# Kernel tuning notes

Measured on AMD Instinct MI355X. Metric: run time of the kernel, lower is better.

## Reference

```python
import jax, jax.numpy as jnp
from jax import lax
import numpy as np

N, C, H, W = 8, 128, 96, 96
G, K = 8, 3                      # groups, kernel_size
GC = C // G                      # group channels = 16
STRIDE, PAD, DIL = 1, 1, 1
OFFSET_SCALE = 1.0
OM_DIM = int(np.ceil(G * K * K * 3 / 8) * 8)   # 216 (== G*K*K*3, no padding)
GN_EPS = 1e-5


def setup_inputs() -> dict:
    key = jax.random.key(0)
    ks = jax.random.split(key, 7)
    inp = {
        "input": jax.random.normal(ks[0], (N, C, H, W), dtype=jnp.float32),
        # depthwise conv (Conv2d groups=C): OIHW with I=1
        "dw_w": jax.random.normal(ks[1], (C, 1, K, K), dtype=jnp.float32) * 0.1,
        "dw_b": jax.random.normal(ks[2], (C,), dtype=jnp.float32) * 0.05,
        # GroupNorm(num_groups=1) affine params
        "gn_w": jnp.ones((C,), dtype=jnp.float32),
        "gn_b": jnp.zeros((C,), dtype=jnp.float32),
        # offset_mask Linear (module zero-inits; use small random for a meaningful test)
        "om_w": jax.random.normal(ks[3], (OM_DIM, C), dtype=jnp.float32) * 0.02,
        "om_b": jax.random.normal(ks[4], (OM_DIM,), dtype=jnp.float32) * 0.02,
    }
    return inp


def _dcnv4_forward(x, dw_w, dw_b, gn_w, gn_b, om_w, om_b):
    # x: (N, C, H, W)
    # ---- offset/mask branch: depthwise conv -> GroupNorm(1) -> GELU -> Linear
    x1 = lax.conv_general_dilated(
        x, dw_w, window_strides=(1, 1), padding=[(1, 1), (1, 1)],
        feature_group_count=C, dimension_numbers=("NCHW", "OIHW", "NCHW"))
    x1 = x1 + dw_b[None, :, None, None]
    mu = jnp.mean(x1, axis=(1, 2, 3), keepdims=True)
    var = jnp.var(x1, axis=(1, 2, 3), keepdims=True)
    x1 = (x1 - mu) * lax.rsqrt(var + GN_EPS)
    x1 = x1 * gn_w[None, :, None, None] + gn_b[None, :, None, None]
    x1 = jax.nn.gelu(x1, approximate=False)
    x1 = jnp.transpose(x1, (0, 2, 3, 1))                     # (N,H,W,C)
    om = jnp.einsum("nhwc,oc->nhwo", x1, om_w) + om_b        # (N,H,W,216)

    K2 = K * K
    om = om[..., : G * K2 * 3].reshape(N, H, W, G, K2 * 3)
    offs = om[..., : 2 * K2].reshape(N, H, W, G, K2, 2)      # (dx, dy) per point
    mask = om[..., 2 * K2:]                                  # (N,H,W,G,K2), no softmax in DCNv4

    # ---- sampling locations (pixel coords in the unpadded input, zeros outside)
    ky, kx = jnp.meshgrid(jnp.arange(K), jnp.arange(K), indexing="ij")
    base_y = ((ky - (K - 1) / 2.0) * DIL).reshape(-1).astype(jnp.float32)  # (K2,)
    base_x = ((kx - (K - 1) / 2.0) * DIL).reshape(-1).astype(jnp.float32)
    ctr_y = jnp.arange(H, dtype=jnp.float32) * STRIDE - PAD + DIL * (K - 1) / 2.0
    ctr_x = jnp.arange(W, dtype=jnp.float32) * STRIDE - PAD + DIL * (K - 1) / 2.0
    loc_y = ctr_y[None, :, None, None, None] + (base_y + offs[..., 1]) * OFFSET_SCALE
    loc_x = ctr_x[None, None, :, None, None] + (base_x + offs[..., 0]) * OFFSET_SCALE

    # ---- grouped bilinear gather
    xv = jnp.transpose(x, (0, 2, 3, 1)).reshape(N, H, W, G, GC)   # values, channels-last
    y0 = jnp.floor(loc_y)
    x0 = jnp.floor(loc_x)
    ly = loc_y - y0
    lx = loc_x - x0
    y0i = y0.astype(jnp.int32)
    x0i = x0.astype(jnp.int32)
    n_idx = jnp.arange(N)[:, None, None, None, None]
    g_idx = jnp.arange(G)[None, None, None, :, None]

    def gather(yi, xi):
        valid = (yi >= 0) & (yi < H) & (xi >= 0) & (xi < W)
        yc = jnp.clip(yi, 0, H - 1)
        xc = jnp.clip(xi, 0, W - 1)
        v = xv[n_idx, yc, xc, g_idx]                 # (N,H,W,G,K2,GC)
        return v * valid[..., None].astype(xv.dtype)

    samp = (gather(y0i,     x0i)     * ((1 - ly) * (1 - lx))[..., None]
          + gather(y0i,     x0i + 1) * ((1 - ly) * lx)[..., None]
          + gather(y0i + 1, x0i)     * (ly * (1 - lx))[..., None]
          + gather(y0i + 1, x0i + 1) * (ly * lx)[..., None])

    out = jnp.sum(samp * mask[..., None], axis=4)    # (N,H,W,G,GC)
    out = out.reshape(N, H, W, C)
    return jnp.transpose(out, (0, 3, 1, 2))          # (N,C,H,W)


def reference(input, dw_w, dw_b, gn_w, gn_b, om_w, om_b):
    return _dcnv4_forward(input, dw_w, dw_b, gn_w, gn_b, om_w, om_b)
```

## Files before the change

kernel.cpp:

```cpp
#include <hip/hip_runtime.h>
#include <hip/hip_bf16.h>

#define N_   8
#define C_   128
#define H_   96
#define W_   96
#define G_   8
#define GC_  16
#define HW_  (H_ * W_)
#define CHW_ (C_ * HW_)
#define OM_  216
#define OMP_ 224
#define OMROWS2_ 112
#define EPS_ 1e-5f
#define BLKS_PER_N_ 192
#define PW_  100
#define PPLANE_ (PW_ * PW_ * GC_)

typedef short bf16x8 __attribute__((ext_vector_type(8)));
typedef float f32x4 __attribute__((ext_vector_type(4)));

#if __has_builtin(__builtin_amdgcn_fdot2_f32_bf16)
#define HAVE_DOT2_ 1
typedef __bf16 bf16x2 __attribute__((ext_vector_type(2)));
static __device__ __forceinline__ bf16x2 u2bf2(unsigned int u) {
  union { unsigned int i; bf16x2 v; } c;
  c.i = u;
  return c.v;
}
#else
#define HAVE_DOT2_ 0
#endif

static __device__ __forceinline__ unsigned short f2bf(float f) {
  unsigned int u = __float_as_uint(f);
  unsigned int r = (u + 0x7fffu + ((u >> 16) & 1u)) >> 16;
  return (unsigned short)r;
}
static __device__ __forceinline__ unsigned int pk_bf2(float lo, float hi) {
  __hip_bfloat162 h = __float22bfloat162_rn(make_float2(lo, hi));
  union { __hip_bfloat162 h; unsigned int u; } c;
  c.h = h;
  return c.u;
}
static __device__ __forceinline__ float lo_bf(unsigned int u) {
  return __uint_as_float(u << 16);
}
static __device__ __forceinline__ float hi_bf(unsigned int u) {
  return __uint_as_float(u & 0xffff0000u);
}

static __device__ __forceinline__ float fast_gelu(float z) {
  float s = z * 0.70710678118654752f;
  float as = fabsf(s);
  float t = __builtin_amdgcn_rcpf(fmaf(0.3275911f, as, 1.0f));
  float e = __expf(-as * as);
  float inner = fmaf(fmaf(fmaf(fmaf(1.061405429f, t, -1.453152027f), t,
                               1.421413741f), t, -0.284496736f), t, 0.254829592f);
  float y = fmaf(-inner * t, e, 1.0f);
  float erf_s = copysignf(y, s);
  float hz = 0.5f * z;
  return fmaf(hz, erf_s, hz);
}

static __device__ __forceinline__ void loadrow5(float dst[2][5],
                                                const float* __restrict__ xp0,
                                                const float* __restrict__ xp1,
                                                int hh, int w0) {
  bool vy = (hh >= 0) & (hh < H_);
#pragma unroll
  for (int j = 0; j < 5; ++j) {
    int ww = w0 - 1 + j;
    bool v = vy & (ww >= 0) & (ww < W_);
    dst[0][j] = v ? xp0[hh * W_ + ww] : 0.0f;
    dst[1][j] = v ? xp1[hh * W_ + ww] : 0.0f;
  }
}

__global__ __launch_bounds__(256) void k_front(const float* __restrict__ x,
                                               const float* __restrict__ dw_w,
                                               const float* __restrict__ dw_b,
                                               unsigned short* __restrict__ xgb,
                                               unsigned short* __restrict__ x1b,
                                               float2* __restrict__ partials) {
  __shared__ unsigned int lds_c[384 * 9];
  __shared__ unsigned int lds_a[384 * 9];
  __shared__ float ls[4], lq[4];

  int tx = threadIdx.x;
  int ty = threadIdx.y;
  int tid = ty * 32 + tx;
  int hb = blockIdx.x;
  int g  = blockIdx.y;
  int n  = blockIdx.z;
  int h0 = hb * 4;
  int w0 = tx * 3;

  const int c0 = g * 16 + 2 * ty;
  float wk[2][9];
  const float* wp = dw_w + c0 * 9;
#pragma unroll
  for (int j = 0; j < 9; ++j) {
    wk[0][j] = wp[j];
    wk[1][j] = wp[9 + j];
  }
  float bias[2] = {dw_b[c0], dw_b[c0 + 1]};

  const float* xp0 = x + ((size_t)(n * C_ + c0)) * HW_;
  const float* xp1 = xp0 + HW_;

  float s = 0.0f, q = 0.0f;

  float rr[3][2][5];
  loadrow5(rr[0], xp0, xp1, h0 - 1, w0);
  loadrow5(rr[1], xp0, xp1, h0,     w0);

#pragma unroll
  for (int r = 0; r < 4; ++r) {
    const int sA = r % 3;
    const int sB = (r + 1) % 3;
    const int sC = (r + 2) % 3;
    loadrow5(rr[sC], xp0, xp1, h0 + r + 1, w0);

#pragma unroll
    for (int j = 0; j < 3; ++j) {
      float acc0 = bias[0], acc1 = bias[1];
#pragma unroll
      for (int dx = 0; dx < 3; ++dx) {
        acc0 = fmaf(rr[sA][0][j + dx], wk[0][0 + dx], acc0);
        acc1 = fmaf(rr[sA][1][j + dx], wk[1][0 + dx], acc1);
        acc0 = fmaf(rr[sB][0][j + dx], wk[0][3 + dx], acc0);
        acc1 = fmaf(rr[sB][1][j + dx], wk[1][3 + dx], acc1);
        acc0 = fmaf(rr[sC][0][j + dx], wk[0][6 + dx], acc0);
        acc1 = fmaf(rr[sC][1][j + dx], wk[1][6 + dx], acc1);
      }
      float cen0 = rr[sB][0][j + 1];
      float cen1 = rr[sB][1][j + 1];
      s += acc0 + acc1;
      q = fmaf(acc0, acc0, q);
      q = fmaf(acc1, acc1, q);
      int pxl = r * 96 + w0 + j;
      lds_a[pxl * 9 + ty] = pk_bf2(acc0, acc1);
      lds_c[pxl * 9 + ty] = pk_bf2(cen0, cen1);
    }
  }
  __syncthreads();

  for (int i = tid; i < 384; i += 256) {
    int row = i / 96;
    int col = i - row * 96;
    unsigned int wc[8], wa[8];
#pragma unroll
    for (int k = 0; k < 8; ++k) {
      wc[k] = lds_c[i * 9 + k];
      wa[k] = lds_a[i * 9 + k];
    }
    unsigned int* xg = (unsigned int*)xgb + (size_t)(n * G_ + g) * (PPLANE_ / 2)
                       + ((h0 + row + 2) * PW_ + (col + 2)) * 8;
    uint4 c01 = {wc[0], wc[1], wc[2], wc[3]};
    uint4 c23 = {wc[4], wc[5], wc[6], wc[7]};
    *(uint4*)xg = c01;
    *(uint4*)(xg + 4) = c23;
    int p = (h0 + row) * W_ + col;
    unsigned int* xb = (unsigned int*)x1b + ((size_t)n * HW_ + p) * 64 + g * 8;
    uint4 a01 = {wa[0], wa[1], wa[2], wa[3]};
    uint4 a23 = {wa[4], wa[5], wa[6], wa[7]};
    *(uint4*)xb = a01;
    *(uint4*)(xb + 4) = a23;
  }

#pragma unroll
  for (int o = 32; o > 0; o >>= 1) {
    s += __shfl_down(s, o);
    q += __shfl_down(q, o);
  }
  int lane = tid & 63;
  int wv = tid >> 6;
  if (lane == 0) { ls[wv] = s; lq[wv] = q; }
  __syncthreads();
  if (tid == 0) {
    int bid = hb + 24 * g + BLKS_PER_N_ * n;
    partials[bid] = make_float2(ls[0] + ls[1] + ls[2] + ls[3],
                                lq[0] + lq[1] + lq[2] + lq[3]);
  }
}

__global__ __launch_bounds__(256) void k_prep(const float* __restrict__ om_w,
                                              const float* __restrict__ om_b,
                                              unsigned short* __restrict__ A,
                                              float* __restrict__ biasp,
                                              unsigned short* __restrict__ xgb) {
  int b = blockIdx.x;
  int tid = threadIdx.x;
  if (b < 112) {
    int idx = b * 256 + tid;
    int o = idx >> 7;
    int cix = idx & 127;
    int g = o / 28;
    int k = o - g * 28;
    float v = (k < 27) ? om_w[(g * 27 + k) * C_ + cix] : 0.0f;
    A[idx] = f2bf(v);
    if (cix == 0) biasp[o] = (k < 27) ? om_b[g * 27 + k] : 0.0f;
  } else {
    int gid = (b - 112) * 256 + tid;
    const int NBORD = 64 * 784;
    for (int id = gid; id < NBORD; id += 80 * 256) {
      int plane = id / 784;
      int r = id - plane * 784;
      int row, col;
      if (r < 400) {
        int qq = r / 100;
        row = (qq < 2) ? qq : qq + 96;
        col = r - qq * 100;
      } else {
        int r2 = r - 400;
        int qq = r2 >> 2;
        int c4 = r2 & 3;
        row = 2 + qq;
        col = (c4 < 2) ? c4 : c4 + 96;
      }
      uint4* dst = (uint4*)(xgb + (size_t)plane * PPLANE_ + (row * PW_ + col) * GC_);
      uint4 z = {0, 0, 0, 0};
      dst[0] = z;
      dst[1] = z;
    }
  }
}

static __device__ __forceinline__ void pref_af(bf16x8 (&af)[4],
                                               const unsigned short* __restrict__ A,
                                               int ot, int l16, int quad) {
  const unsigned short* Ap = A + (ot * 16 + l16) * C_ + quad * 8;
#pragma unroll
  for (int kk = 0; kk < 4; ++kk) af[kk] = *(const bf16x8*)(Ap + kk * 32);
}

__global__ __launch_bounds__(256) void k_gemm_mfma(const unsigned short* __restrict__ Bt,
                                                   const unsigned short* __restrict__ A,
                                                   const float* __restrict__ biasp,
                                                   const float2* __restrict__ partials,
                                                   const float* __restrict__ gn_w,
                                                   const float* __restrict__ gn_b,
                                                   unsigned int* __restrict__ om2) {
  __shared__ unsigned short Bl[32 * 136];
  __shared__ alignas(16) float s_bias[OMP_];
  __shared__ float ls[4], lq[4];
  int tid = threadIdx.x;
  int pb = blockIdx.x;
  int n = blockIdx.y;
  int p0 = pb * 32;

  const unsigned short* src = Bt + ((size_t)n * HW_ + p0) * C_;
  int col = tid & 15;
  int row0 = tid >> 4;
  uint4 raw0 = *(const uint4*)(src + row0 * C_ + col * 8);
  uint4 raw1 = *(const uint4*)(src + (16 + row0) * C_ + col * 8);
  int cbase = col * 8;
  float gw8[8], gb8[8];
#pragma unroll
  for (int j = 0; j < 8; ++j) {
    gw8[j] = gn_w[cbase + j];
    gb8[j] = gn_b[cbase + j];
  }
  if (tid < OMP_ / 4) {
    ((float4*)s_bias)[tid] = ((const float4*)biasp)[tid];
  }

  {
    float s = 0.0f, q = 0.0f;
    if (tid < BLKS_PER_N_) {
      float2 v = partials[n * BLKS_PER_N_ + tid];
      s = v.x;
      q = v.y;
    }
#pragma unroll
    for (int o = 32; o > 0; o >>= 1) {
      s += __shfl_down(s, o);
      q += __shfl_down(q, o);
    }
    int lane = tid & 63;
    int wv = tid >> 6;
    if (lane == 0) { ls[wv] = s; lq[wv] = q; }
  }
  __syncthreads();

  float sum = ls[0] + ls[1] + ls[2] + ls[3];
  float ssq = lq[0] + lq[1] + lq[2] + lq[3];
  const float inv = 1.0f / (float)CHW_;
  float mean = sum * inv;
  float var = ssq * inv - mean * mean;
  float rstd = rsqrtf(var + EPS_);
  float a8[8], b8[8];
#pragma unroll
  for (int j = 0; j < 8; ++j) {
    a8[j] = rstd * gw8[j];
    b8[j] = gb8[j] - mean * rstd * gw8[j];
  }

  {
    uint4 raws[2] = {raw0, raw1};
#pragma unroll
    for (int i = 0; i < 2; ++i) {
      int row = row0 + i * 16;
      unsigned int d[4] = {raws[i].x, raws[i].y, raws[i].z, raws[i].w};
      unsigned int od[4];
#pragma unroll
      for (int t = 0; t < 4; ++t) {
        float v0 = lo_bf(d[t]);
        float v1 = hi_bf(d[t]);
        float z0 = fmaf(v0, a8[2 * t], b8[2 * t]);
        float z1 = fmaf(v1, a8[2 * t + 1], b8[2 * t + 1]);
        od[t] = pk_bf2(fast_gelu(z0), fast_gelu(z1));
      }
      uint4 packed = {od[0], od[1], od[2], od[3]};
      *(uint4*)(&Bl[row * 136 + col * 8]) = packed;
    }
  }
  __syncthreads();

  int wave = tid >> 6;
  int lane = tid & 63;
  int quad = lane >> 4;
  int l16 = lane & 15;
  int pixhalf = wave & 1;
  int othalf = wave >> 1;
  int prow = pixhalf * 16 + l16;

  bf16x8 bfrag[4];
#pragma unroll
  for (int kk = 0; kk < 4; ++kk)
    bfrag[kk] = *(const bf16x8*)(&Bl[prow * 136 + kk * 32 + quad * 8]);

  int p = p0 + prow;
  int base = othalf * 7;

#define COMP_(AF, OT)                                                          \
  {                                                                            \
    f32x4 acc = {0.f, 0.f, 0.f, 0.f};                                          \
    _Pragma("unroll")                                                          \
    for (int kk = 0; kk < 4; ++kk)                                             \
      acc = __builtin_amdgcn_mfma_f32_16x16x32_bf16(AF[kk], bfrag[kk], acc,    \
                                                    0, 0, 0);                  \
    int o0 = (OT) * 16 + quad * 4;                                             \
    float4 bv = *(const float4*)(&s_bias[o0]);                                 \
    unsigned int pk0 = pk_bf2(acc[0] + bv.x, acc[1] + bv.y);                   \
    unsigned int pk1 = pk_bf2(acc[2] + bv.z, acc[3] + bv.w);                   \
    unsigned int* Cp = om2 + ((size_t)n * OMROWS2_ + (o0 >> 1)) * HW_ + p;     \
    Cp[0] = pk0;                                                               \
    Cp[HW_] = pk1;                                                             \
  }

  bf16x8 af0[4], af1[4];
  pref_af(af0, A, base + 0, l16, quad);
  pref_af(af1, A, base + 1, l16, quad);
  COMP_(af0, base + 0);
  pref_af(af0, A, base + 2, l16, quad);
  COMP_(af1, base + 1);
  pref_af(af1, A, base + 3, l16, quad);
  COMP_(af0, base + 2);
  pref_af(af0, A, base + 4, l16, quad);
  COMP_(af1, base + 3);
  pref_af(af1, A, base + 5, l16, quad);
  COMP_(af0, base + 4);
  pref_af(af0, A, base + 6, l16, quad);
  COMP_(af1, base + 5);
  COMP_(af0, base + 6);
#undef COMP_
}

__global__ __launch_bounds__(256) void k_sample(const unsigned short* __restrict__ xgb,
                                                const unsigned int* __restrict__ om2,
                                                float* __restrict__ out) {
  __shared__ int4 s_wa[9 * 64];

  int tid = threadIdx.x;
  int ord = blockIdx.x;
  int n = ord & 7;
  int t2 = ord >> 3;
  int g = t2 & 7;
  int pb = t2 >> 3;
  int p0 = pb * 64;

  const unsigned int* omb = om2 + ((size_t)n * OMROWS2_ + g * 14) * HW_ + p0;
  for (int j = tid; j < 576; j += 256) {
    int pt = j >> 6;
    int px = j & 63;
    int p = p0 + px;
    int h = p / W_;
    int w = p - h * W_;
    unsigned int od = omb[pt * HW_ + px];
    float offx = lo_bf(od);
    float offy = hi_bf(od);
    unsigned int md = omb[(9 + (pt >> 1)) * HW_ + px];
    float m = (pt & 1) ? hi_bf(md) : lo_bf(md);
    float locy = (float)(h + pt / 3 - 1) + offy;
    float locx = (float)(w + pt % 3 - 1) + offx;
    float y0f = floorf(locy);
    float x0f = floorf(locx);
    float ly = locy - y0f;
    float lx = locx - x0f;
    int y0 = (int)y0f;
    int x0 = (int)x0f;
    y0 = min(max(y0, -2), 96);
    x0 = min(max(x0, -2), 96);
    float t0 = (1.0f - ly) * m;
    float t1 = ly * m;
    float u0 = 1.0f - lx;
    int4 wa;
    wa.x = (int)pk_bf2(t0 * u0, t1 * u0);
    wa.y = (int)pk_bf2(t0 * lx, t1 * lx);
    wa.z = ((y0 + 2) * PW_ + (x0 + 2)) * GC_;
    wa.w = wa.z + PW_ * GC_;
    s_wa[j] = wa;
  }
  __syncthreads();

  int px_l = tid >> 2;
  int sub = tid & 3;
  int rowhalf = sub >> 1;
  int chunk = sub & 1;
  int p = p0 + px_l;
  const unsigned short* xbb = xgb + (size_t)(n * G_ + g) * PPLANE_;

  float acc[8] = {0, 0, 0, 0, 0, 0, 0, 0};
#pragma unroll
  for (int pt = 0; pt < 9; ++pt) {
    int4 wa = s_wa[pt * 64 + px_l];
    unsigned int aw = (unsigned int)(rowhalf ? wa.y : wa.x);
    uint4 r0 = *(const uint4*)(xbb + wa.z + sub * 8);
    uint4 r1 = *(const uint4*)(xbb + wa.w + sub * 8);
    unsigned int d0[4] = {r0.x, r0.y, r0.z, r0.w};
    unsigned int d1[4] = {r1.x, r1.y, r1.z, r1.w};
#if HAVE_DOT2_
    bf16x2 a2 = u2bf2(aw);
#pragma unroll
    for (int t = 0; t < 4; ++t) {
      unsigned int blo = __builtin_amdgcn_perm(d1[t], d0[t], 0x05040100u);
      unsigned int bhi = __builtin_amdgcn_perm(d1[t], d0[t], 0x07060302u);
      acc[2 * t]     = __builtin_amdgcn_fdot2_f32_bf16(a2, u2bf2(blo), acc[2 * t], false);
      acc[2 * t + 1] = __builtin_amdgcn_fdot2_f32_bf16(a2, u2bf2(bhi), acc[2 * t + 1], false);
    }
#else
    float w0 = lo_bf(aw);
    float w1 = hi_bf(aw);
#pragma unroll
    for (int t = 0; t < 4; ++t) {
      acc[2 * t]     = fmaf(w0, lo_bf(d0[t]), acc[2 * t]);
      acc[2 * t + 1] = fmaf(w0, hi_bf(d0[t]), acc[2 * t + 1]);
      acc[2 * t]     = fmaf(w1, lo_bf(d1[t]), acc[2 * t]);
      acc[2 * t + 1] = fmaf(w1, hi_bf(d1[t]), acc[2 * t + 1]);
    }
#endif
  }

#pragma unroll
  for (int i = 0; i < 8; ++i) acc[i] += __shfl_xor(acc[i], 2);

  int ch = chunk * 8 + rowhalf * 4;
  float* op = out + ((size_t)(n * C_ + g * GC_ + ch)) * HW_ + p;
#pragma unroll
  for (int r = 0; r < 4; ++r) op[r * HW_] = acc[rowhalf * 4 + r];
}

extern "C" void kernel_launch(void* const* d_in, const int* in_sizes, int n_in,
                              void* d_out, int out_size, void* d_ws, size_t ws_size,
                              hipStream_t stream) {
  const float* x    = (const float*)d_in[0];
  const float* dw_w = (const float*)d_in[1];
  const float* dw_b = (const float*)d_in[2];
  const float* gn_w = (const float*)d_in[3];
  const float* gn_b = (const float*)d_in[4];
  const float* om_w = (const float*)d_in[5];
  const float* om_b = (const float*)d_in[6];
  float* out = (float*)d_out;

  unsigned short* xgb = (unsigned short*)d_ws;
  unsigned short* x1b = xgb + (size_t)64 * PPLANE_;
  unsigned int* om2 = (unsigned int*)(x1b + (size_t)N_ * CHW_);
  float* stats = (float*)(om2 + (size_t)N_ * OMROWS2_ * HW_);
  float2* partials = (float2*)(stats + 16);
  unsigned short* Abf = (unsigned short*)(partials + N_ * BLKS_PER_N_);
  float* biasp = (float*)(Abf + OMP_ * C_);

  k_prep<<<192, 256, 0, stream>>>(om_w, om_b, Abf, biasp, xgb);
  k_front<<<dim3(24, G_, N_), dim3(32, 8), 0, stream>>>(
      x, dw_w, dw_b, xgb, x1b, partials);
  k_gemm_mfma<<<dim3(HW_ / 32, N_), 256, 0, stream>>>(
      x1b, Abf, biasp, partials, gn_w, gn_b, om2);
  k_sample<<<9216, 256, 0, stream>>>(xgb, om2, out);
}
```

Measured before the change: 180.4 us.

## Merge prep into front kernel and software-pipeline sampling gathers

Folds the weight-conversion and border-zeroing prep work into the front depthwise-conv kernel as extra blocks, saving one kernel launch and its serialization. The front kernel switches to a 1D grid with flattened index decoding. In the sampling kernel, the gathers for the next sampling point are issued before computing the current one, to hide global load latency. It also adds a launch-bounds occupancy hint of 4 on k_sample, which adds register pressure from the double-buffered registers.

```diff
diff --git a/kernel.cpp b/kernel.cpp
--- a/kernel.cpp
+++ b/kernel.cpp
@@ -82,17 +82,62 @@
                                                const float* __restrict__ dw_b,
                                                unsigned short* __restrict__ xgb,
                                                unsigned short* __restrict__ x1b,
-                                               float2* __restrict__ partials) {
+                                               float2* __restrict__ partials,
+                                               const float* __restrict__ om_w,
+                                               const float* __restrict__ om_b,
+                                               unsigned short* __restrict__ A,
+                                               float* __restrict__ biasp) {
+  int fb = blockIdx.x;
+  int tid = threadIdx.x;
+
+  if (fb >= N_ * BLKS_PER_N_) {
+    int pb2 = fb - N_ * BLKS_PER_N_;
+    if (pb2 < 112) {
+      int idx = pb2 * 256 + tid;
+      int o = idx >> 7;
+      int cix = idx & 127;
+      int g = o / 28;
+      int k = o - g * 28;
+      float v = (k < 27) ? om_w[(g * 27 + k) * C_ + cix] : 0.0f;
+      A[idx] = f2bf(v);
+      if (cix == 0) biasp[o] = (k < 27) ? om_b[g * 27 + k] : 0.0f;
+    } else {
+      int gid = (pb2 - 112) * 256 + tid;
+      const int NBORD = 64 * 784;
+      for (int id = gid; id < NBORD; id += 80 * 256) {
+        int plane = id / 784;
+        int r = id - plane * 784;
+        int row, col;
+        if (r < 400) {
+          int qq = r / 100;
+          row = (qq < 2) ? qq : qq + 96;
+          col = r - qq * 100;
+        } else {
+          int r2 = r - 400;
+          int qq = r2 >> 2;
+          int c4 = r2 & 3;
+          row = 2 + qq;
+          col = (c4 < 2) ? c4 : c4 + 96;
+        }
+        uint4* dst = (uint4*)(xgb + (size_t)plane * PPLANE_ + (row * PW_ + col) * GC_);
+        uint4 z = {0, 0, 0, 0};
+        dst[0] = z;
+        dst[1] = z;
+      }
+    }
+    return;
+  }
+
   __shared__ unsigned int lds_c[384 * 9];
   __shared__ unsigned int lds_a[384 * 9];
   __shared__ float ls[4], lq[4];
 
-  int tx = threadIdx.x;
-  int ty = threadIdx.y;
-  int tid = ty * 32 + tx;
-  int hb = blockIdx.x;
-  int g  = blockIdx.y;
-  int n  = blockIdx.z;
+  int tx = tid & 31;
+  int ty = tid >> 5;
+  int n   = fb / BLKS_PER_N_;
+  int rem = fb - n * BLKS_PER_N_;
+  int g   = rem / 24;
+  int hb  = rem - g * 24;
   int h0 = hb * 4;
   int w0 = tx * 3;
 
@@ -179,51 +224,8 @@
   if (lane == 0) { ls[wv] = s; lq[wv] = q; }
   __syncthreads();
   if (tid == 0) {
-    int bid = hb + 24 * g + BLKS_PER_N_ * n;
-    partials[bid] = make_float2(ls[0] + ls[1] + ls[2] + ls[3],
-                                lq[0] + lq[1] + lq[2] + lq[3]);
-  }
-}
-
-__global__ __launch_bounds__(256) void k_prep(const float* __restrict__ om_w,
-                                              const float* __restrict__ om_b,
-                                              unsigned short* __restrict__ A,
-                                              float* __restrict__ biasp,
-                                              unsigned short* __restrict__ xgb) {
-  int b = blockIdx.x;
-  int tid = threadIdx.x;
-  if (b < 112) {
-    int idx = b * 256 + tid;
-    int o = idx >> 7;
-    int cix = idx & 127;
-    int g = o / 28;
-    int k = o - g * 28;
-    float v = (k < 27) ? om_w[(g * 27 + k) * C_ + cix] : 0.0f;
-    A[idx] = f2bf(v);
-    if (cix == 0) biasp[o] = (k < 27) ? om_b[g * 27 + k] : 0.0f;
-  } else {
-    int gid = (b - 112) * 256 + tid;
-    const int NBORD = 64 * 784;
-    for (int id = gid; id < NBORD; id += 80 * 256) {
-      int plane = id / 784;
-      int r = id - plane * 784;
-      int row, col;
-      if (r < 400) {
-        int qq = r / 100;
-        row = (qq < 2) ? qq : qq + 96;
-        col = r - qq * 100;
-      } else {
-        int r2 = r - 400;
-        int qq = r2 >> 2;
-        int c4 = r2 & 3;
-        row = 2 + qq;
-        col = (c4 < 2) ? c4 : c4 + 96;
-      }
-      uint4* dst = (uint4*)(xgb + (size_t)plane * PPLANE_ + (row * PW_ + col) * GC_);
-      uint4 z = {0, 0, 0, 0};
-      dst[0] = z;
-      dst[1] = z;
-    }
+    partials[fb] = make_float2(ls[0] + ls[1] + ls[2] + ls[3],
+                               lq[0] + lq[1] + lq[2] + lq[3]);
   }
 }
 
@@ -368,9 +370,9 @@
 #undef COMP_
 }
 
-__global__ __launch_bounds__(256) void k_sample(const unsigned short* __restrict__ xgb,
-                                                const unsigned int* __restrict__ om2,
-                                                float* __restrict__ out) {
+__global__ __launch_bounds__(256, 4) void k_sample(const unsigned short* __restrict__ xgb,
+                                                   const unsigned int* __restrict__ om2,
+                                                   float* __restrict__ out) {
   __shared__ int4 s_wa[9 * 64];
 
   int tid = threadIdx.x;
@@ -423,12 +425,22 @@
   const unsigned short* xbb = xgb + (size_t)(n * G_ + g) * PPLANE_;
 
   float acc[8] = {0, 0, 0, 0, 0, 0, 0, 0};
+
+  int4 wa = s_wa[px_l];
+  uint4 r0 = *(const uint4*)(xbb + wa.z + sub * 8);
+  uint4 r1 = *(const uint4*)(xbb + wa.w + sub * 8);
+
 #pragma unroll
   for (int pt = 0; pt < 9; ++pt) {
-    int4 wa = s_wa[pt * 64 + px_l];
+    int4 wa_n;
+    uint4 r0n, r1n;
+    if (pt < 8) {
+      wa_n = s_wa[(pt + 1) * 64 + px_l];
+      r0n = *(const uint4*)(xbb + wa_n.z + sub * 8);
+      r1n = *(const uint4*)(xbb + wa_n.w + sub * 8);
+    }
+
     unsigned int aw = (unsigned int)(rowhalf ? wa.y : wa.x);
-    uint4 r0 = *(const uint4*)(xbb + wa.z + sub * 8);
-    uint4 r1 = *(const uint4*)(xbb + wa.w + sub * 8);
     unsigned int d0[4] = {r0.x, r0.y, r0.z, r0.w};
     unsigned int d1[4] = {r1.x, r1.y, r1.z, r1.w};
 #if HAVE_DOT2_
@@ -451,6 +463,11 @@
       acc[2 * t + 1] = fmaf(w1, hi_bf(d1[t]), acc[2 * t + 1]);
     }
 #endif
+    if (pt < 8) {
+      wa = wa_n;
+      r0 = r0n;
+      r1 = r1n;
+    }
   }
 
 #pragma unroll
@@ -482,9 +499,8 @@
   unsigned short* Abf = (unsigned short*)(partials + N_ * BLKS_PER_N_);
   float* biasp = (float*)(Abf + OMP_ * C_);
 
-  k_prep<<<192, 256, 0, stream>>>(om_w, om_b, Abf, biasp, xgb);
-  k_front<<<dim3(24, G_, N_), dim3(32, 8), 0, stream>>>(
-      x, dw_w, dw_b, xgb, x1b, partials);
+  k_front<<<N_ * BLKS_PER_N_ + 192, 256, 0, stream>>>(
+      x, dw_w, dw_b, xgb, x1b, partials, om_w, om_b, Abf, biasp);
   k_gemm_mfma<<<dim3(HW_ / 32, N_), 256, 0, stream>>>(
       x1b, Abf, biasp, partials, gn_w, gn_b, om2);
   k_sample<<<9216, 256, 0, stream>>>(xgb, om2, out);
```

Result: no change. 183.6 us (+1.7%).
